# Performance work log

Measured on AMD Instinct MI355X. Metric: run time of the kernel, lower is better.

Reference implementation:

```python
import jax, jax.numpy as jnp
import numpy as np

D, H, E, K = 1024, 1024, 8, 2  # model dim, expert hidden dim, n_experts, top_k


def setup_inputs() -> dict:
    key = jax.random.key(0)
    ks = jax.random.split(key, 5)
    s = lambda k, shape, scale: jax.random.normal(k, shape, dtype=jnp.float32) * scale
    return {
        "input_batch": s(ks[0], (2, 512, D), 1.0),
        "router_w": s(ks[1], (D, E), D ** -0.5),
        "w_in": s(ks[2], (E, D, H), D ** -0.5),
        "b_in": jnp.zeros((E, H), jnp.float32),
        "w_out": s(ks[3], (E, H, D), H ** -0.5),
        "b_out": jnp.zeros((E, D), jnp.float32),
    }


def _moe(x, router_w, w_in, b_in, w_out, b_out):
    B, S, Dm = x.shape
    T = B * S
    x2 = x.reshape(T, Dm)
    # router: per-token logit scores over experts
    logits = x2 @ router_w                                # [T, E]
    probs = jax.nn.softmax(logits, axis=-1)
    # sampler: top-k experts per token
    top_p, top_e = jax.lax.top_k(probs, K)                # [T, K]
    flat_e = top_e.reshape(-1)                            # [N] with N = T*K
    flat_p = top_p.reshape(-1)
    tok = jnp.repeat(jnp.arange(T), K)                    # owning token of each dispatch row
    # sort dispatched rows by expert id (expert_sorted_indices in the original)
    order = jnp.argsort(flat_e)
    se, sp, st = flat_e[order], flat_p[order], tok[order]
    xd = x2[st]                                           # [N, D] gathered dispatch
    N = xd.shape[0]
    # per-expert 2-layer MLP; loop over the small fixed expert set with masking
    h = jnp.zeros((N, H), x.dtype)
    for e in range(E):
        m = (se == e)[:, None]
        h = h + jnp.where(m, jax.nn.gelu(xd @ w_in[e] + b_in[e]), 0.0)
    y = jnp.zeros((N, Dm), x.dtype)
    for e in range(E):
        m = (se == e)[:, None]
        y = y + jnp.where(m, h @ w_out[e] + b_out[e], 0.0)
    # weighted scatter-combine (index_add in the original)
    y = y * sp[:, None]
    out = jnp.zeros((T, Dm), x.dtype).at[st].add(y)
    return out.reshape(B, S, Dm)


def reference(input_batch, router_w, w_in, b_in, w_out, b_out):
    return _moe(input_batch, router_w, w_in, b_in, w_out, b_out)
```

## Files before the change

kernel.cpp:

```cpp
#include <hip/hip_runtime.h>
#include <hip/hip_bf16.h>

#define DM 1024
#define HD 1024
#define NE 8
#define NT 1024
#define NR 2048
#define BM 64
#define BN 64
#define BKK 64
#define LDK 72
#define MT_MAX 40
#define PN_MAX (MT_MAX * BM)
#define NBLK (MT_MAX * (HD / BN))
#define NXCD 8

typedef __attribute__((ext_vector_type(8))) short short8;
typedef __attribute__((ext_vector_type(4))) float f32x4;

typedef const __attribute__((address_space(1))) void* gas_ptr;
typedef __attribute__((address_space(3))) void* las_ptr;

__device__ __forceinline__ void glds16(const void* g, void* l) {
    __builtin_amdgcn_global_load_lds((gas_ptr)g, (las_ptr)l, 16, 0, 0);
}

__device__ __forceinline__ float gelu_tanh(float x) {
    float x3 = x * x * x;
    return 0.5f * x * (1.0f + tanhf(0.7978845608028654f * (x + 0.044715f * x3)));
}

__global__ void moe_router(const float* __restrict__ x, const float* __restrict__ rw,
                           int* __restrict__ e_sel, float* __restrict__ p_sel) {
    int t = blockIdx.x;
    int lane = threadIdx.x;
    const float* xr = x + (size_t)t * DM;
    float acc[NE];
#pragma unroll
    for (int e = 0; e < NE; ++e) acc[e] = 0.0f;
    for (int d = lane; d < DM; d += 64) {
        float xv = xr[d];
        const float* r = rw + (size_t)d * NE;
#pragma unroll
        for (int e = 0; e < NE; ++e) acc[e] += xv * r[e];
    }
#pragma unroll
    for (int e = 0; e < NE; ++e) {
#pragma unroll
        for (int off = 32; off > 0; off >>= 1) acc[e] += __shfl_xor(acc[e], off);
    }
    if (lane == 0) {
        float m = acc[0];
#pragma unroll
        for (int e = 1; e < NE; ++e) m = fmaxf(m, acc[e]);
        float p[NE];
        float s = 0.0f;
#pragma unroll
        for (int e = 0; e < NE; ++e) { p[e] = __expf(acc[e] - m); s += p[e]; }
        float inv = 1.0f / s;
        int i0 = 0;
#pragma unroll
        for (int e = 1; e < NE; ++e) if (p[e] > p[i0]) i0 = e;
        int i1 = (i0 == 0) ? 1 : 0;
#pragma unroll
        for (int e = 0; e < NE; ++e) if (e != i1 && e != i0 && p[e] > p[i1]) i1 = e;
        e_sel[2 * t + 0] = i0;
        e_sel[2 * t + 1] = i1;
        p_sel[2 * t + 0] = p[i0] * inv;
        p_sel[2 * t + 1] = p[i1] * inv;
    }
}

__global__ void moe_route_pack(const int* __restrict__ e_sel, int* __restrict__ meta,
                               int* __restrict__ sorted_tok, int* __restrict__ pos_of_row) {
    __shared__ int scnt[NE];
    __shared__ int soff[NE];
    int tid = threadIdx.x;
    if (tid < NE) scnt[tid] = 0;
    __syncthreads();
    for (int i = tid; i < NR; i += 256) atomicAdd(&scnt[e_sel[i]], 1);
    __syncthreads();
    if (tid == 0) {
        int off = 0, tc = 0;
        for (int e = 0; e < NE; ++e) {
            soff[e] = off;
            meta[8 + e] = off;
            int nt = (scnt[e] + BM - 1) / BM;
            for (int t = 0; t < nt; ++t) meta[16 + tc++] = e;
            off += nt * BM;
            scnt[e] = 0;
        }
        for (; tc < MT_MAX; ++tc) meta[16 + tc] = -1;
    }
    __syncthreads();
    for (int i = tid; i < PN_MAX; i += 256) sorted_tok[i] = -1;
    __syncthreads();
    for (int i = tid; i < NR; i += 256) {
        int e = e_sel[i];
        int r = atomicAdd(&scnt[e], 1);
        int pos = soff[e] + r;
        sorted_tok[pos] = i >> 1;
        pos_of_row[i] = pos;
    }
}

__global__ __launch_bounds__(256) void moe_gather(const float* __restrict__ x,
                                                  const int* __restrict__ sorted_tok,
                                                  __hip_bfloat16* __restrict__ xg) {
    int pos = blockIdx.x;
    int t = sorted_tok[pos];
    int j = threadIdx.x * 4;
    ushort4 u;
    if (t >= 0) {
        float4 f = *(const float4*)(x + (size_t)t * DM + j);
        __hip_bfloat16 b0 = __float2bfloat16(f.x), b1 = __float2bfloat16(f.y);
        __hip_bfloat16 b2 = __float2bfloat16(f.z), b3 = __float2bfloat16(f.w);
        u.x = *(unsigned short*)&b0; u.y = *(unsigned short*)&b1;
        u.z = *(unsigned short*)&b2; u.w = *(unsigned short*)&b3;
    } else {
        u.x = u.y = u.z = u.w = 0;
    }
    *(ushort4*)((unsigned short*)xg + (size_t)pos * DM + j) = u;
}

__global__ __launch_bounds__(256) void moe_transpose(const float* __restrict__ w_in,
                                                     const float* __restrict__ w_out,
                                                     __hip_bfloat16* __restrict__ wt1,
                                                     __hip_bfloat16* __restrict__ wt2) {
    int ty = blockIdx.y;
    const float* src = (ty < 8 ? w_in : w_out) + (size_t)(ty & 7) * DM * HD;
    unsigned short* dst = (unsigned short*)(ty < 8 ? wt1 : wt2) + (size_t)(ty & 7) * DM * HD;
    int k0 = (blockIdx.x >> 4) * 64, n0 = (blockIdx.x & 15) * 64;
    __shared__ float ts[64][65];
    int r = threadIdx.x >> 4;
    int c = (threadIdx.x & 15) * 4;
#pragma unroll
    for (int i = 0; i < 4; ++i) {
        int rr = r + 16 * i;
        float4 f = *(const float4*)(src + (size_t)(k0 + rr) * HD + n0 + c);
        ts[rr][c] = f.x; ts[rr][c + 1] = f.y; ts[rr][c + 2] = f.z; ts[rr][c + 3] = f.w;
    }
    __syncthreads();
#pragma unroll
    for (int i = 0; i < 4; ++i) {
        int rn = r + 16 * i;
        __hip_bfloat16 b0 = __float2bfloat16(ts[c][rn]);
        __hip_bfloat16 b1 = __float2bfloat16(ts[c + 1][rn]);
        __hip_bfloat16 b2 = __float2bfloat16(ts[c + 2][rn]);
        __hip_bfloat16 b3 = __float2bfloat16(ts[c + 3][rn]);
        ushort4 u;
        u.x = *(unsigned short*)&b0; u.y = *(unsigned short*)&b1;
        u.z = *(unsigned short*)&b2; u.w = *(unsigned short*)&b3;
        *(ushort4*)(dst + (size_t)(n0 + rn) * DM + k0 + c) = u;
    }
}

template <int EPI>
__global__ __launch_bounds__(256, 3) void moe_gemm_async(const __hip_bfloat16* __restrict__ A,
                                                         const __hip_bfloat16* __restrict__ Bt,
                                                         const float* __restrict__ bias,
                                                         const int* __restrict__ meta,
                                                         __hip_bfloat16* __restrict__ Hout,
                                                         float* __restrict__ Yout) {
    int bid = blockIdx.x;
    int swz = (bid % NXCD) * (NBLK / NXCD) + bid / NXCD;
    int mt = swz >> 4;
    int nb = swz & 15;
    int e = meta[16 + mt];
    if (e < 0) return;

    __shared__ __align__(16) unsigned char smem[3 * 16384];

    int tid = threadIdx.x;
    int wid = tid >> 6, lane = tid & 63;
    int wm = wid >> 1, wn = wid & 1;

    const unsigned short* Ab = (const unsigned short*)A + (size_t)mt * BM * DM;
    const unsigned short* Bb = (const unsigned short*)Bt + (size_t)e * DM * HD + (size_t)nb * BN * DM;

    int srow = wid * 16 + (lane >> 3);
    int s_log = (lane & 7) ^ (lane >> 3);
    const unsigned short* agp0 = Ab + (size_t)srow * DM + s_log * 8;
    const unsigned short* agp1 = agp0 + 8 * DM;
    const unsigned short* bgp0 = Bb + (size_t)srow * DM + s_log * 8;
    const unsigned short* bgp1 = bgp0 + 8 * DM;

    auto ISSUE = [&](int b, int kt) {
        unsigned char* sa = &smem[b * 16384 + wid * 2048];
        unsigned char* sb = &smem[b * 16384 + 8192 + wid * 2048];
        glds16(agp0 + kt * BKK, sa);
        glds16(agp1 + kt * BKK, sa + 1024);
        glds16(bgp0 + kt * BKK, sb);
        glds16(bgp1 + kt * BKK, sb + 1024);
    };

    int r16 = lane & 15, g = lane >> 4, l7 = lane & 7;
    int aoff[2][2], boff[2][2];
#pragma unroll
    for (int kk = 0; kk < 2; ++kk)
#pragma unroll
        for (int f = 0; f < 2; ++f) {
            int sw = (((kk << 2) + g) ^ l7) << 4;
            aoff[kk][f] = (wm * 32 + r16 + 16 * f) * 128 + sw;
            boff[kk][f] = (wn * 32 + r16 + 16 * f) * 128 + sw;
        }

    f32x4 acc[2][2] = {};

    ISSUE(0, 0);
    ISSUE(1, 1);
    ISSUE(2, 2);

#pragma unroll
    for (int kt = 0; kt < 16; ++kt) {
        if (kt <= 13)      asm volatile("s_waitcnt vmcnt(8)" ::: "memory");
        else if (kt == 14) asm volatile("s_waitcnt vmcnt(4)" ::: "memory");
        else               asm volatile("s_waitcnt vmcnt(0)" ::: "memory");
        asm volatile("s_barrier" ::: "memory");
        const unsigned char* sa = &smem[(kt % 3) * 16384];
        const unsigned char* sb = sa + 8192;
#pragma unroll
        for (int kk = 0; kk < 2; ++kk) {
            short8 a0 = *(const short8*)(sa + aoff[kk][0]);
            short8 a1 = *(const short8*)(sa + aoff[kk][1]);
            short8 b0 = *(const short8*)(sb + boff[kk][0]);
            short8 b1 = *(const short8*)(sb + boff[kk][1]);
            acc[0][0] = __builtin_amdgcn_mfma_f32_16x16x32_bf16(a0, b0, acc[0][0], 0, 0, 0);
            acc[0][1] = __builtin_amdgcn_mfma_f32_16x16x32_bf16(a0, b1, acc[0][1], 0, 0, 0);
            acc[1][0] = __builtin_amdgcn_mfma_f32_16x16x32_bf16(a1, b0, acc[1][0], 0, 0, 0);
            acc[1][1] = __builtin_amdgcn_mfma_f32_16x16x32_bf16(a1, b1, acc[1][1], 0, 0, 0);
        }
        asm volatile("s_barrier" ::: "memory");
        if (kt + 3 < 16) ISSUE(kt % 3, kt + 3);
    }

    int row0 = mt * BM + wm * 32 + ((lane >> 4) << 2);
    int col0 = nb * BN + wn * 32 + (lane & 15);
    const float* be = bias + (size_t)e * HD;
#pragma unroll
    for (int fm = 0; fm < 2; ++fm) {
#pragma unroll
        for (int fn = 0; fn < 2; ++fn) {
            int c = col0 + fn * 16;
            float bv = be[c];
#pragma unroll
            for (int r = 0; r < 4; ++r) {
                int rr = row0 + fm * 16 + r;
                float v = acc[fm][fn][r] + bv;
                if (EPI == 0) {
                    Hout[(size_t)rr * HD + c] = __float2bfloat16(gelu_tanh(v));
                } else {
                    Yout[(size_t)rr * HD + c] = v;
                }
            }
        }
    }
}

__global__ __launch_bounds__(256) void moe_combine(const float* __restrict__ y,
                                                   const float* __restrict__ p_sel,
                                                   const int* __restrict__ pos_of_row,
                                                   float* __restrict__ out) {
    int t = blockIdx.x;
    int j = threadIdx.x * 4;
    int q0 = pos_of_row[2 * t], q1 = pos_of_row[2 * t + 1];
    float p0 = p_sel[2 * t], p1 = p_sel[2 * t + 1];
    float4 a = *(const float4*)(y + (size_t)q0 * DM + j);
    float4 b = *(const float4*)(y + (size_t)q1 * DM + j);
    float4 o;
    o.x = p0 * a.x + p1 * b.x;
    o.y = p0 * a.y + p1 * b.y;
    o.z = p0 * a.z + p1 * b.z;
    o.w = p0 * a.w + p1 * b.w;
    *(float4*)(out + (size_t)t * DM + j) = o;
}

template <int EPI>
__global__ __launch_bounds__(256) void moe_gemm(const __hip_bfloat16* __restrict__ A,
                                                const float* __restrict__ W,
                                                const float* __restrict__ bias,
                                                const int* __restrict__ meta,
                                                __hip_bfloat16* __restrict__ Hout,
                                                float* __restrict__ Yout) {
    int mt = blockIdx.y;
    int e = meta[16 + mt];
    if (e < 0) return;
    int nb = blockIdx.x;
    __shared__ __align__(16) __hip_bfloat16 As[2][BM][LDK];
    __shared__ __align__(16) __hip_bfloat16 Bs[2][BN][LDK];
    int tid = threadIdx.x;
    int wid = tid >> 6, lane = tid & 63;
    int wm = wid >> 1, wn = wid & 1;
    const __hip_bfloat16* Ab = A + (size_t)mt * BM * DM;
    const float* Wb = W + (size_t)e * DM * HD + (size_t)nb * BN;
    uint4 ra[2];
    float4 rb[4];
    auto GLOAD = [&](int kt) {
#pragma unroll
        for (int i = 0; i < 2; ++i) {
            int c = tid + 256 * i;
            int row = c >> 3, col8 = c & 7;
            ra[i] = *(const uint4*)((const unsigned short*)Ab + (size_t)row * DM + kt * BKK + col8 * 8);
        }
#pragma unroll
        for (int i = 0; i < 4; ++i) {
            int c = tid + 256 * i;
            int kr = c >> 4, c4 = c & 15;
            rb[i] = *(const float4*)(Wb + (size_t)(kt * BKK + kr) * HD + c4 * 4);
        }
    };
    auto STORE = [&](int b) {
#pragma unroll
        for (int i = 0; i < 2; ++i) {
            int c = tid + 256 * i;
            int row = c >> 3, col8 = c & 7;
            *(uint4*)&As[b][row][col8 * 8] = ra[i];
        }
#pragma unroll
        for (int i = 0; i < 4; ++i) {
            int c = tid + 256 * i;
            int kr = c >> 4, c4 = c & 15;
            Bs[b][c4 * 4 + 0][kr] = __float2bfloat16(rb[i].x);
            Bs[b][c4 * 4 + 1][kr] = __float2bfloat16(rb[i].y);
            Bs[b][c4 * 4 + 2][kr] = __float2bfloat16(rb[i].z);
            Bs[b][c4 * 4 + 3][kr] = __float2bfloat16(rb[i].w);
        }
    };
    f32x4 acc[2][2] = {};
    GLOAD(0);
    STORE(0);
    __syncthreads();
    int buf = 0;
    const int NK = DM / BKK;
    for (int kt = 0; kt < NK; ++kt) {
        if (kt + 1 < NK) GLOAD(kt + 1);
#pragma unroll
        for (int kk = 0; kk < 2; ++kk) {
            int kb = kk * 32 + (lane >> 4) * 8;
            short8 a0 = *(const short8*)&As[buf][wm * 32 + (lane & 15)][kb];
            short8 a1 = *(const short8*)&As[buf][wm * 32 + 16 + (lane & 15)][kb];
            short8 b0 = *(const short8*)&Bs[buf][wn * 32 + (lane & 15)][kb];
            short8 b1 = *(const short8*)&Bs[buf][wn * 32 + 16 + (lane & 15)][kb];
            acc[0][0] = __builtin_amdgcn_mfma_f32_16x16x32_bf16(a0, b0, acc[0][0], 0, 0, 0);
            acc[0][1] = __builtin_amdgcn_mfma_f32_16x16x32_bf16(a0, b1, acc[0][1], 0, 0, 0);
            acc[1][0] = __builtin_amdgcn_mfma_f32_16x16x32_bf16(a1, b0, acc[1][0], 0, 0, 0);
            acc[1][1] = __builtin_amdgcn_mfma_f32_16x16x32_bf16(a1, b1, acc[1][1], 0, 0, 0);
        }
        if (kt + 1 < NK) {
            STORE(buf ^ 1);
            __syncthreads();
            buf ^= 1;
        }
    }
    int row0 = mt * BM + wm * 32 + ((lane >> 4) << 2);
    int col0 = nb * BN + wn * 32 + (lane & 15);
    const float* be = bias + (size_t)e * HD;
#pragma unroll
    for (int fm = 0; fm < 2; ++fm) {
#pragma unroll
        for (int fn = 0; fn < 2; ++fn) {
            int c = col0 + fn * 16;
            float bv = be[c];
#pragma unroll
            for (int r = 0; r < 4; ++r) {
                int rr = row0 + fm * 16 + r;
                float v = acc[fm][fn][r] + bv;
                if (EPI == 0) {
                    Hout[(size_t)rr * HD + c] = __float2bfloat16(gelu_tanh(v));
                } else {
                    Yout[(size_t)rr * HD + c] = v;
                }
            }
        }
    }
}

extern "C" void kernel_launch(void* const* d_in, const int* in_sizes, int n_in,
                              void* d_out, int out_size, void* d_ws, size_t ws_size,
                              hipStream_t stream) {
    const float* x     = (const float*)d_in[0];
    const float* rw    = (const float*)d_in[1];
    const float* w_in  = (const float*)d_in[2];
    const float* b_in  = (const float*)d_in[3];
    const float* w_out = (const float*)d_in[4];
    const float* b_out = (const float*)d_in[5];
    float* out = (float*)d_out;

    char* ws = (char*)d_ws;
    int*   e_sel      = (int*)ws;
    float* p_sel      = (float*)(ws + 8 * 1024);
    int*   meta       = (int*)(ws + 16 * 1024);
    int*   sorted_tok = (int*)(ws + 17 * 1024);
    int*   pos_of_row = (int*)(ws + 27 * 1024);

    const size_t SZ_X  = (size_t)PN_MAX * DM * 2;
    const size_t SZ_Y  = (size_t)PN_MAX * DM * 4;
    const size_t SZ_WT = (size_t)NE * DM * HD * 2;

    __hip_bfloat16* xg  = (__hip_bfloat16*)(ws + 64 * 1024);
    __hip_bfloat16* h   = (__hip_bfloat16*)(ws + 64 * 1024 + SZ_X);
    __hip_bfloat16* wt1 = (__hip_bfloat16*)(ws + 64 * 1024 + 2 * SZ_X);
    float*          y   = (float*)wt1;
    __hip_bfloat16* wt2 = (__hip_bfloat16*)(ws + 64 * 1024 + 2 * SZ_X + SZ_WT);

    const size_t NEED_FULL = 64 * 1024 + 2 * SZ_X + 2 * SZ_WT;
    const size_t NEED_R2   = 64 * 1024 + SZ_X + SZ_Y;

    if (ws_size >= NEED_FULL) {
        moe_router<<<NT, 64, 0, stream>>>(x, rw, e_sel, p_sel);
        moe_route_pack<<<1, 256, 0, stream>>>(e_sel, meta, sorted_tok, pos_of_row);
        moe_gather<<<PN_MAX, 256, 0, stream>>>(x, sorted_tok, xg);
        moe_transpose<<<dim3(256, 16), 256, 0, stream>>>(w_in, w_out, wt1, wt2);
        moe_gemm_async<0><<<NBLK, 256, 0, stream>>>(xg, wt1, b_in, meta, h, nullptr);
        moe_gemm_async<1><<<NBLK, 256, 0, stream>>>(h, wt2, b_out, meta, nullptr, y);
        moe_combine<<<NT, 256, 0, stream>>>(y, p_sel, pos_of_row, out);
    } else if (ws_size >= NEED_R2) {
        __hip_bfloat16* h2  = (__hip_bfloat16*)(ws + 64 * 1024);
        __hip_bfloat16* xg2 = (__hip_bfloat16*)(ws + 64 * 1024 + SZ_X);
        float* y2           = (float*)xg2;
        moe_router<<<NT, 64, 0, stream>>>(x, rw, e_sel, p_sel);
        moe_route_pack<<<1, 256, 0, stream>>>(e_sel, meta, sorted_tok, pos_of_row);
        moe_gather<<<PN_MAX, 256, 0, stream>>>(x, sorted_tok, xg2);
        dim3 grid(HD / BN, MT_MAX);
        moe_gemm<0><<<grid, 256, 0, stream>>>(xg2, w_in, b_in, meta, h2, nullptr);
        moe_gemm<1><<<grid, 256, 0, stream>>>(h2, w_out, b_out, meta, nullptr, y2);
        moe_combine<<<NT, 256, 0, stream>>>(y2, p_sel, pos_of_row, out);
    }
}
```

Before: 68.55 us.

## Enlarge expert GEMM tiles to 128x128 with double-buffered async LDS loads

Replaces the 64x64 MoE GEMM tile with a 128x128 tile in which each wave computes a 4x4 grid of MFMA fragments. Routing metadata now pads each expert's rows to multiples of 128. The aim is higher data reuse per LDS load and fewer blocks re-reading weights. The costs are more padding rows, fewer blocks in the grid (possible underfill of the CUs), a two-stage pipeline instead of three, and lower occupancy. The fallback path is adapted to the new metadata granularity.

Result: slower. 75.72 us (+10.5%).

```diff
diff --git a/kernel.cpp b/kernel.cpp
--- a/kernel.cpp
+++ b/kernel.cpp
@@ -6,14 +6,14 @@
 #define NE 8
 #define NT 1024
 #define NR 2048
-#define BM 64
-#define BN 64
 #define BKK 64
+#define BM2 128
+#define BN2 128
+#define MT2 24
+#define PN2 (MT2 * BM2)
+#define NBLK2 (MT2 * (HD / BN2))
+#define NXCD 8
 #define LDK 72
-#define MT_MAX 40
-#define PN_MAX (MT_MAX * BM)
-#define NBLK (MT_MAX * (HD / BN))
-#define NXCD 8
 
 typedef __attribute__((ext_vector_type(8))) short short8;
 typedef __attribute__((ext_vector_type(4))) float f32x4;
@@ -24,6 +24,8 @@
 __device__ __forceinline__ void glds16(const void* g, void* l) {
     __builtin_amdgcn_global_load_lds((gas_ptr)g, (las_ptr)l, 16, 0, 0);
 }
+
+#define WAITV(n) asm volatile("s_waitcnt vmcnt(" #n ")" ::: "memory")
 
 __device__ __forceinline__ float gelu_tanh(float x) {
     float x3 = x * x * x;
@@ -85,15 +87,15 @@
         for (int e = 0; e < NE; ++e) {
             soff[e] = off;
             meta[8 + e] = off;
-            int nt = (scnt[e] + BM - 1) / BM;
+            int nt = (scnt[e] + BM2 - 1) / BM2;
             for (int t = 0; t < nt; ++t) meta[16 + tc++] = e;
-            off += nt * BM;
+            off += nt * BM2;
             scnt[e] = 0;
         }
-        for (; tc < MT_MAX; ++tc) meta[16 + tc] = -1;
-    }
-    __syncthreads();
-    for (int i = tid; i < PN_MAX; i += 256) sorted_tok[i] = -1;
+        for (; tc < MT2; ++tc) meta[16 + tc] = -1;
+    }
+    __syncthreads();
+    for (int i = tid; i < PN2; i += 256) sorted_tok[i] = -1;
     __syncthreads();
     for (int i = tid; i < NR; i += 256) {
         int e = e_sel[i];
@@ -156,91 +158,94 @@
 }
 
 template <int EPI>
-__global__ __launch_bounds__(256, 3) void moe_gemm_async(const __hip_bfloat16* __restrict__ A,
-                                                         const __hip_bfloat16* __restrict__ Bt,
-                                                         const float* __restrict__ bias,
-                                                         const int* __restrict__ meta,
-                                                         __hip_bfloat16* __restrict__ Hout,
-                                                         float* __restrict__ Yout) {
+__global__ __launch_bounds__(256, 2) void moe_gemm_big(const __hip_bfloat16* __restrict__ A,
+                                                       const __hip_bfloat16* __restrict__ Bt,
+                                                       const float* __restrict__ bias,
+                                                       const int* __restrict__ meta,
+                                                       __hip_bfloat16* __restrict__ Hout,
+                                                       float* __restrict__ Yout) {
     int bid = blockIdx.x;
-    int swz = (bid % NXCD) * (NBLK / NXCD) + bid / NXCD;
-    int mt = swz >> 4;
-    int nb = swz & 15;
+    int swz = (bid % NXCD) * (NBLK2 / NXCD) + bid / NXCD;
+    int mt = swz >> 3;
+    int nb = swz & 7;
     int e = meta[16 + mt];
     if (e < 0) return;
 
-    __shared__ __align__(16) unsigned char smem[3 * 16384];
+    __shared__ __align__(16) unsigned char smem[2 * 32768];
 
     int tid = threadIdx.x;
     int wid = tid >> 6, lane = tid & 63;
     int wm = wid >> 1, wn = wid & 1;
 
-    const unsigned short* Ab = (const unsigned short*)A + (size_t)mt * BM * DM;
-    const unsigned short* Bb = (const unsigned short*)Bt + (size_t)e * DM * HD + (size_t)nb * BN * DM;
-
-    int srow = wid * 16 + (lane >> 3);
-    int s_log = (lane & 7) ^ (lane >> 3);
-    const unsigned short* agp0 = Ab + (size_t)srow * DM + s_log * 8;
-    const unsigned short* agp1 = agp0 + 8 * DM;
-    const unsigned short* bgp0 = Bb + (size_t)srow * DM + s_log * 8;
-    const unsigned short* bgp1 = bgp0 + 8 * DM;
+    const unsigned short* Ab = (const unsigned short*)A + (size_t)mt * BM2 * DM;
+    const unsigned short* Bb = (const unsigned short*)Bt + (size_t)e * DM * HD + (size_t)nb * BN2 * DM;
+
+    int lrow = lane >> 3;
+    int s_log = (lane & 7) ^ lrow;
+    const unsigned short* agp[4];
+    const unsigned short* bgp[4];
+#pragma unroll
+    for (int i = 0; i < 4; ++i) {
+        int row = i * 32 + wid * 8 + lrow;
+        agp[i] = Ab + (size_t)row * DM + s_log * 8;
+        bgp[i] = Bb + (size_t)row * DM + s_log * 8;
+    }
 
     auto ISSUE = [&](int b, int kt) {
-        unsigned char* sa = &smem[b * 16384 + wid * 2048];
-        unsigned char* sb = &smem[b * 16384 + 8192 + wid * 2048];
-        glds16(agp0 + kt * BKK, sa);
-        glds16(agp1 + kt * BKK, sa + 1024);
-        glds16(bgp0 + kt * BKK, sb);
-        glds16(bgp1 + kt * BKK, sb + 1024);
+        unsigned char* sa = &smem[b * 32768 + wid * 1024];
+        unsigned char* sb = sa + 16384;
+#pragma unroll
+        for (int i = 0; i < 4; ++i) glds16(agp[i] + kt * BKK, sa + i * 4096);
+#pragma unroll
+        for (int i = 0; i < 4; ++i) glds16(bgp[i] + kt * BKK, sb + i * 4096);
     };
 
     int r16 = lane & 15, g = lane >> 4, l7 = lane & 7;
-    int aoff[2][2], boff[2][2];
+    int aoff[2][4], boff[2][4];
 #pragma unroll
     for (int kk = 0; kk < 2; ++kk)
 #pragma unroll
-        for (int f = 0; f < 2; ++f) {
+        for (int f = 0; f < 4; ++f) {
             int sw = (((kk << 2) + g) ^ l7) << 4;
-            aoff[kk][f] = (wm * 32 + r16 + 16 * f) * 128 + sw;
-            boff[kk][f] = (wn * 32 + r16 + 16 * f) * 128 + sw;
-        }
-
-    f32x4 acc[2][2] = {};
+            aoff[kk][f] = (wm * 64 + f * 16 + r16) * 128 + sw;
+            boff[kk][f] = (wn * 64 + f * 16 + r16) * 128 + sw + 16384;
+        }
+
+    f32x4 acc[4][4] = {};
 
     ISSUE(0, 0);
     ISSUE(1, 1);
-    ISSUE(2, 2);
 
 #pragma unroll
     for (int kt = 0; kt < 16; ++kt) {
-        if (kt <= 13)      asm volatile("s_waitcnt vmcnt(8)" ::: "memory");
-        else if (kt == 14) asm volatile("s_waitcnt vmcnt(4)" ::: "memory");
-        else               asm volatile("s_waitcnt vmcnt(0)" ::: "memory");
+        if (kt <= 14) WAITV(8);
+        else          WAITV(0);
         asm volatile("s_barrier" ::: "memory");
-        const unsigned char* sa = &smem[(kt % 3) * 16384];
-        const unsigned char* sb = sa + 8192;
+        const unsigned char* sm = &smem[(kt & 1) * 32768];
 #pragma unroll
         for (int kk = 0; kk < 2; ++kk) {
-            short8 a0 = *(const short8*)(sa + aoff[kk][0]);
-            short8 a1 = *(const short8*)(sa + aoff[kk][1]);
-            short8 b0 = *(const short8*)(sb + boff[kk][0]);
-            short8 b1 = *(const short8*)(sb + boff[kk][1]);
-            acc[0][0] = __builtin_amdgcn_mfma_f32_16x16x32_bf16(a0, b0, acc[0][0], 0, 0, 0);
-            acc[0][1] = __builtin_amdgcn_mfma_f32_16x16x32_bf16(a0, b1, acc[0][1], 0, 0, 0);
-            acc[1][0] = __builtin_amdgcn_mfma_f32_16x16x32_bf16(a1, b0, acc[1][0], 0, 0, 0);
-            acc[1][1] = __builtin_amdgcn_mfma_f32_16x16x32_bf16(a1, b1, acc[1][1], 0, 0, 0);
+            short8 av[4], bv[4];
+#pragma unroll
+            for (int f = 0; f < 4; ++f) av[f] = *(const short8*)(sm + aoff[kk][f]);
+#pragma unroll
+            for (int f = 0; f < 4; ++f) bv[f] = *(const short8*)(sm + boff[kk][f]);
+#pragma unroll
+            for (int fm = 0; fm < 4; ++fm)
+#pragma unroll
+                for (int fn = 0; fn < 4; ++fn)
+                    acc[fm][fn] = __builtin_amdgcn_mfma_f32_16x16x32_bf16(av[fm], bv[fn], acc[fm][fn], 0, 0, 0);
         }
         asm volatile("s_barrier" ::: "memory");
-        if (kt + 3 < 16) ISSUE(kt % 3, kt + 3);
-    }
-
-    int row0 = mt * BM + wm * 32 + ((lane >> 4) << 2);
-    int col0 = nb * BN + wn * 32 + (lane & 15);
+        if (kt + 2 < 16) ISSUE(kt & 1, kt + 2);
+    }
+
+    int row0 = mt * BM2 + wm * 64 + g * 4;
+    int col0 = nb * BN2 + wn * 64 + r16;
     const float* be = bias + (size_t)e * HD;
 #pragma unroll
-    for (int fm = 0; fm < 2; ++fm) {
-#pragma unroll
-        for (int fn = 0; fn < 2; ++fn) {
+    for (int fm = 0; fm < 4; ++fm) {
+#pragma unroll
+        for (int fn = 0; fn < 4; ++fn) {
             int c = col0 + fn * 16;
             float bv = be[c];
 #pragma unroll
@@ -250,7 +255,7 @@
                 if (EPI == 0) {
                     Hout[(size_t)rr * HD + c] = __float2bfloat16(gelu_tanh(v));
                 } else {
-                    Yout[(size_t)rr * HD + c] = v;
+                    Yout[(size_t)rr * DM + c] = v;
                 }
             }
         }
@@ -283,16 +288,16 @@
                                                 __hip_bfloat16* __restrict__ Hout,
                                                 float* __restrict__ Yout) {
     int mt = blockIdx.y;
-    int e = meta[16 + mt];
+    int e = meta[16 + (mt >> 1)];
     if (e < 0) return;
     int nb = blockIdx.x;
-    __shared__ __align__(16) __hip_bfloat16 As[2][BM][LDK];
-    __shared__ __align__(16) __hip_bfloat16 Bs[2][BN][LDK];
+    __shared__ __align__(16) __hip_bfloat16 As[2][64][LDK];
+    __shared__ __align__(16) __hip_bfloat16 Bs[2][64][LDK];
     int tid = threadIdx.x;
     int wid = tid >> 6, lane = tid & 63;
     int wm = wid >> 1, wn = wid & 1;
-    const __hip_bfloat16* Ab = A + (size_t)mt * BM * DM;
-    const float* Wb = W + (size_t)e * DM * HD + (size_t)nb * BN;
+    const __hip_bfloat16* Ab = A + (size_t)mt * 64 * DM;
+    const float* Wb = W + (size_t)e * DM * HD + (size_t)nb * 64;
     uint4 ra[2];
     float4 rb[4];
     auto GLOAD = [&](int kt) {
@@ -352,8 +357,8 @@
             buf ^= 1;
         }
     }
-    int row0 = mt * BM + wm * 32 + ((lane >> 4) << 2);
-    int col0 = nb * BN + wn * 32 + (lane & 15);
+    int row0 = mt * 64 + wm * 32 + ((lane >> 4) << 2);
+    int col0 = nb * 64 + wn * 32 + (lane & 15);
     const float* be = bias + (size_t)e * HD;
 #pragma unroll
     for (int fm = 0; fm < 2; ++fm) {
@@ -391,10 +396,10 @@
     float* p_sel      = (float*)(ws + 8 * 1024);
     int*   meta       = (int*)(ws + 16 * 1024);
     int*   sorted_tok = (int*)(ws + 17 * 1024);
-    int*   pos_of_row = (int*)(ws + 27 * 1024);
-
-    const size_t SZ_X  = (size_t)PN_MAX * DM * 2;
-    const size_t SZ_Y  = (size_t)PN_MAX * DM * 4;
+    int*   pos_of_row = (int*)(ws + 32 * 1024);
+
+    const size_t SZ_X  = (size_t)PN2 * DM * 2;
+    const size_t SZ_Y  = (size_t)PN2 * DM * 4;
     const size_t SZ_WT = (size_t)NE * DM * HD * 2;
 
     __hip_bfloat16* xg  = (__hip_bfloat16*)(ws + 64 * 1024);
@@ -404,26 +409,21 @@
     __hip_bfloat16* wt2 = (__hip_bfloat16*)(ws + 64 * 1024 + 2 * SZ_X + SZ_WT);
 
     const size_t NEED_FULL = 64 * 1024 + 2 * SZ_X + 2 * SZ_WT;
-    const size_t NEED_R2   = 64 * 1024 + SZ_X + SZ_Y;
-
+    const size_t NEED_FB   = 64 * 1024 + 2 * SZ_X + SZ_Y;
+
+    moe_router<<<NT, 64, 0, stream>>>(x, rw, e_sel, p_sel);
+    moe_route_pack<<<1, 256, 0, stream>>>(e_sel, meta, sorted_tok, pos_of_row);
+    moe_gather<<<PN2, 256, 0, stream>>>(x, sorted_tok, xg);
     if (ws_size >= NEED_FULL) {
-        moe_router<<<NT, 64, 0, stream>>>(x, rw, e_sel, p_sel);
-        moe_route_pack<<<1, 256, 0, stream>>>(e_sel, meta, sorted_tok, pos_of_row);
-        moe_gather<<<PN_MAX, 256, 0, stream>>>(x, sorted_tok, xg);
         moe_transpose<<<dim3(256, 16), 256, 0, stream>>>(w_in, w_out, wt1, wt2);
-        moe_gemm_async<0><<<NBLK, 256, 0, stream>>>(xg, wt1, b_in, meta, h, nullptr);
-        moe_gemm_async<1><<<NBLK, 256, 0, stream>>>(h, wt2, b_out, meta, nullptr, y);
+        moe_gemm_big<0><<<NBLK2, 256, 0, stream>>>(xg, wt1, b_in, meta, h, nullptr);
+        moe_gemm_big<1><<<NBLK2, 256, 0, stream>>>(h, wt2, b_out, meta, nullptr, y);
         moe_combine<<<NT, 256, 0, stream>>>(y, p_sel, pos_of_row, out);
-    } else if (ws_size >= NEED_R2) {
-        __hip_bfloat16* h2  = (__hip_bfloat16*)(ws + 64 * 1024);
-        __hip_bfloat16* xg2 = (__hip_bfloat16*)(ws + 64 * 1024 + SZ_X);
-        float* y2           = (float*)xg2;
-        moe_router<<<NT, 64, 0, stream>>>(x, rw, e_sel, p_sel);
-        moe_route_pack<<<1, 256, 0, stream>>>(e_sel, meta, sorted_tok, pos_of_row);
-        moe_gather<<<PN_MAX, 256, 0, stream>>>(x, sorted_tok, xg2);
-        dim3 grid(HD / BN, MT_MAX);
-        moe_gemm<0><<<grid, 256, 0, stream>>>(xg2, w_in, b_in, meta, h2, nullptr);
-        moe_gemm<1><<<grid, 256, 0, stream>>>(h2, w_out, b_out, meta, nullptr, y2);
+    } else if (ws_size >= NEED_FB) {
+        float* y2 = (float*)(ws + 64 * 1024 + 2 * SZ_X);
+        dim3 grid(HD / 64, PN2 / 64);
+        moe_gemm<0><<<grid, 256, 0, stream>>>(xg, w_in, b_in, meta, h, nullptr);
+        moe_gemm<1><<<grid, 256, 0, stream>>>(h, w_out, b_out, meta, nullptr, y2);
         moe_combine<<<NT, 256, 0, stream>>>(y2, p_sel, pos_of_row, out);
     }
 }
```
